# Optimization experiments

Measured on AMD Instinct MI355X. Metric: run time of the kernel, lower is better.

Reference implementation:

```python
import jax, jax.numpy as jnp
import numpy as np

B, N_IN, D_IN = 64, 2048, 16
N_OUT, D_OUT = 32, 32
ROUTINGS = 3
EPS = 1e-7


def squash(s, axis=-1):
    # standard CapsNet squash: s * ||s||^2 / (1 + ||s||^2) / ||s||
    sq_norm = jnp.sum(jnp.square(s), axis=axis, keepdims=True)
    scale = sq_norm / (1.0 + sq_norm) / jnp.sqrt(sq_norm + EPS)
    return s * scale


def setup_inputs() -> dict:
    key = jax.random.key(0)
    k1, k2 = jax.random.split(key)
    inputs = jax.random.normal(k1, (B, N_IN, D_IN), dtype=jnp.float32)
    # glorot-uniform-ish scale for [N_out, N_in, D_out, D_in] weight
    limit = np.sqrt(6.0 / (D_IN + D_OUT)).astype(np.float32)
    weight_matrix = jax.random.uniform(k2, (N_OUT, N_IN, D_OUT, D_IN), dtype=jnp.float32,
                                       minval=-limit, maxval=limit)
    return {"inputs": inputs, "weight_matrix": weight_matrix}


def reference(inputs, weight_matrix):
    # u_hat[b,o,i,d] = W[o,i,d,k] @ x[b,i,k]  (replaces tile + map_fn matmul)
    u_hat = jnp.einsum('oidk,bik->boid', weight_matrix, inputs)  # [B, N_out, N_in, D_out]
    b_logits = jnp.zeros((inputs.shape[0], N_OUT, 1, N_IN), dtype=u_hat.dtype)
    v = None
    for r in range(ROUTINGS):
        c = jax.nn.softmax(b_logits, axis=1)                      # softmax over output capsules
        s = jnp.einsum('boli,boid->bold', c, u_hat)               # [B, N_out, 1, D_out]
        v = squash(s)
        if r < ROUTINGS - 1:
            b_logits = b_logits + jnp.einsum('bold,boid->boli', v, u_hat)
    return jnp.squeeze(v, axis=2)                                 # [B, N_out, D_out]
```

## Files before the change

kernel.cpp:

```cpp
#include <hip/hip_runtime.h>

#define B_    64
#define NI    2048
#define DK    16
#define NO    32
#define DOUT  32
#define EPSQ  1e-7f

__device__ __forceinline__ unsigned pack2_bf16(float a, float b) {
    unsigned ua = __float_as_uint(a);
    unsigned ub = __float_as_uint(b);
    ua = (ua + 0x7fffu + ((ua >> 16) & 1u)) >> 16;
    ub = (ub + 0x7fffu + ((ub >> 16) & 1u)) >> 16;
    return ua | (ub << 16);
}
__device__ __forceinline__ float bf_lo(unsigned w) { return __uint_as_float(w << 16); }
__device__ __forceinline__ float bf_hi(unsigned w) { return __uint_as_float(w & 0xffff0000u); }


constexpr int WSTRIDE = 516;

__global__ __launch_bounds__(512)
void compute_uhat(const float* __restrict__ x, const float* __restrict__ W,
                  ushort* __restrict__ U)
{
    __shared__ float Ws[NO * WSTRIDE];
    __shared__ float xs[B_ * DK];
    const int i = blockIdx.x;
    const int t = threadIdx.x;

    if (t < 256) {
        const int b = t >> 2, k4 = t & 3;
        float4 v = *(const float4*)(x + ((size_t)b * NI + i) * DK + k4 * 4);
        *(float4*)&xs[b * DK + k4 * 4] = v;
    }

    #pragma unroll
    for (int jj = 0; jj < 8; ++jj) {
        const int p  = t + 512 * jj;
        const int oo = p >> 7;
        const int cc = p & 127;
        float4 v = ((const float4*)(W + ((size_t)oo * NI + i) * (DOUT * DK)))[cc];
        *(float4*)&Ws[oo * WSTRIDE + cc * 4] = v;
    }

    const int o  = t & 31;
    const int q  = (t >> 5) & 7;
    const int bh = t >> 8;

    __syncthreads();

    float w[64];
    {
        const float* wr = &Ws[o * WSTRIDE + q * 64];
        #pragma unroll
        for (int m = 0; m < 16; ++m) {
            float4 v = *(const float4*)(wr + 4 * m);
            w[4*m+0] = v.x; w[4*m+1] = v.y; w[4*m+2] = v.z; w[4*m+3] = v.w;
        }
    }

    const int j = q >> 1, half = q & 1;

    for (int bb = 0; bb < 32; ++bb) {
        const int b = bh * 32 + bb;
        const float4* xv = (const float4*)&xs[b * DK];
        const float4 x0 = xv[0], x1 = xv[1], x2 = xv[2], x3 = xv[3];

        float acc[4];
        #pragma unroll
        for (int dl = 0; dl < 4; ++dl) {
            const float* wr = &w[dl * 16];
            float a;
            a  = wr[0]  * x0.x + wr[1]  * x0.y + wr[2]  * x0.z + wr[3]  * x0.w;
            a += wr[4]  * x1.x + wr[5]  * x1.y + wr[6]  * x1.z + wr[7]  * x1.w;
            a += wr[8]  * x2.x + wr[9]  * x2.y + wr[10] * x2.z + wr[11] * x2.w;
            a += wr[12] * x3.x + wr[13] * x3.y + wr[14] * x3.z + wr[15] * x3.w;
            acc[dl] = a;
        }

        uint2 pk;
        pk.x = pack2_bf16(acc[0], acc[1]);
        pk.y = pack2_bf16(acc[2], acc[3]);
        const size_t off = ((((size_t)b * NI + i) * 4 + j) * NO + o) * 8 + half * 4;
        *(uint2*)(U + off) = pk;
    }
}

template<bool UNI>
__device__ __forceinline__ void proc_i(const uint4* cr, const float* vs, float* sacc)
{
    unsigned cw[16];
    #pragma unroll
    for (int jj = 0; jj < 4; ++jj) {
        cw[4*jj+0] = cr[jj].x; cw[4*jj+1] = cr[jj].y;
        cw[4*jj+2] = cr[jj].z; cw[4*jj+3] = cr[jj].w;
    }

    if (UNI) {
        #pragma unroll
        for (int m = 0; m < 16; ++m) {
            const int d0 = (m >> 2) * 8 + (m & 3) * 2;
            sacc[d0]     += bf_lo(cw[m]);
            sacc[d0 + 1] += bf_hi(cw[m]);
        }
    } else {
        float l0 = 0.f, l1 = 0.f, l2 = 0.f, l3 = 0.f;
        #pragma unroll
        for (int m = 0; m < 16; m += 4) {
            const int d0 = (m >> 2) * 8;
            l0 = fmaf(vs[d0+0], bf_lo(cw[m+0]), l0);
            l0 = fmaf(vs[d0+1], bf_hi(cw[m+0]), l0);
            l1 = fmaf(vs[d0+2], bf_lo(cw[m+1]), l1);
            l1 = fmaf(vs[d0+3], bf_hi(cw[m+1]), l1);
            l2 = fmaf(vs[d0+4], bf_lo(cw[m+2]), l2);
            l2 = fmaf(vs[d0+5], bf_hi(cw[m+2]), l2);
            l3 = fmaf(vs[d0+6], bf_lo(cw[m+3]), l3);
            l3 = fmaf(vs[d0+7], bf_hi(cw[m+3]), l3);
        }
        const float logit = (l0 + l1) + (l2 + l3);

        float mx = logit;
        #pragma unroll
        for (int msk = 16; msk >= 1; msk >>= 1) mx = fmaxf(mx, __shfl_xor(mx, msk));
        const float e = __expf(logit - mx);
        float ssum = e;
        #pragma unroll
        for (int msk = 16; msk >= 1; msk >>= 1) ssum += __shfl_xor(ssum, msk);
        const float c = e / ssum;

        #pragma unroll
        for (int m = 0; m < 16; ++m) {
            const int d0 = (m >> 2) * 8 + (m & 3) * 2;
            sacc[d0]     = fmaf(c, bf_lo(cw[m]), sacc[d0]);
            sacc[d0 + 1] = fmaf(c, bf_hi(cw[m]), sacc[d0 + 1]);
        }
    }
}

constexpr int BPB = 16;
constexpr int NIB = NI / BPB / 16;

template<bool UNI>
__global__ __launch_bounds__(256)
void routing_stream(const ushort* __restrict__ U, const float* __restrict__ Vsum,
                    float* __restrict__ s_out)
{
    __shared__ float sblk[NO * DOUT];
    const int t  = threadIdx.x;
    const int b  = blockIdx.x >> 4;
    const int i0 = (blockIdx.x & (BPB - 1)) * (NI / BPB);
    const int o  = t & 31;
    const int hw = t >> 5;

    for (int n = t; n < NO * DOUT; n += 256) sblk[n] = 0.f;

    float vs[DOUT];
    if (!UNI) {
        const float4* vp = (const float4*)(Vsum + ((size_t)b * NO + o) * DOUT);
        #pragma unroll
        for (int m = 0; m < 8; ++m) {
            float4 v = vp[m];
            vs[4*m+0] = v.x; vs[4*m+1] = v.y; vs[4*m+2] = v.z; vs[4*m+3] = v.w;
        }
    }
    float sacc[DOUT];
    #pragma unroll
    for (int d = 0; d < DOUT; ++d) sacc[d] = 0.f;

    __syncthreads();

    const uint4* up = (const uint4*)U + ((size_t)b * NI + i0 + 2 * hw) * (4 * NO) + o;
    const size_t step = (size_t)16 * 4 * NO;

    uint4 cur[8];
    #pragma unroll
    for (int jj = 0; jj < 4; ++jj) {
        cur[jj]     = up[jj * NO];
        cur[4 + jj] = up[4 * NO + jj * NO];
    }
    up += step;

    for (int ii = 0; ii < NIB; ++ii) {
        uint4 nxt[8];
        if (ii + 1 < NIB) {
            #pragma unroll
            for (int jj = 0; jj < 4; ++jj) {
                nxt[jj]     = up[jj * NO];
                nxt[4 + jj] = up[4 * NO + jj * NO];
            }
            up += step;
        }

        proc_i<UNI>(&cur[0], vs, sacc);
        proc_i<UNI>(&cur[4], vs, sacc);

        #pragma unroll
        for (int jj = 0; jj < 8; ++jj) cur[jj] = nxt[jj];
    }

    if (UNI) {
        #pragma unroll
        for (int d = 0; d < DOUT; ++d) sacc[d] *= 0.03125f;
    }

    #pragma unroll
    for (int d = 0; d < DOUT; ++d) sacc[d] += __shfl_xor(sacc[d], 32);

    if ((t & 32) == 0) {
        #pragma unroll
        for (int d = 0; d < DOUT; ++d) atomicAdd(&sblk[o * DOUT + d], sacc[d]);
    }
    __syncthreads();

    float* sp = s_out + (size_t)b * NO * DOUT;
    for (int n = t; n < NO * DOUT; n += 256) atomicAdd(&sp[n], sblk[n]);
}

__global__ __launch_bounds__(256)
void squash_update(const float* __restrict__ s, float* __restrict__ Vsum,
                   float* __restrict__ out, int last)
{
    const int tid  = threadIdx.x;
    const int pair = blockIdx.x * 8 + (tid >> 5);
    const int d    = tid & 31;
    const int idx  = pair * DOUT + d;

    const float val = s[idx];
    float sq = val * val;
    #pragma unroll
    for (int msk = 16; msk >= 1; msk >>= 1) sq += __shfl_xor(sq, msk);

    const float scale = sq / (1.f + sq) * rsqrtf(sq + EPSQ);
    const float v = val * scale;

    if (last) out[idx] = v;
    else      Vsum[idx] += v;
}

constexpr int BTILE  = 16;
constexpr int ITILE  = 32;
constexpr int CHUNKS = NI / ITILE;
constexpr int GB     = B_ / BTILE;
constexpr int WROW   = DOUT * DK + 4;

__global__ __launch_bounds__(512)
void routing_pass(const float* __restrict__ x, const float* __restrict__ W,
                  const float* __restrict__ Vsum, float* __restrict__ s_out)
{
    __shared__ float W_s[NO * WROW];
    const int tid   = threadIdx.x;
    const int o     = tid & 31;
    const int bl    = tid >> 5;
    const int chunk = blockIdx.x & (CHUNKS - 1);
    const int gb    = blockIdx.x / CHUNKS;
    const int b     = gb * BTILE + bl;

    float vs[DOUT];
    {
        const float4* vp = (const float4*)(Vsum + (size_t)(b * NO + o) * DOUT);
        #pragma unroll
        for (int qq = 0; qq < 8; ++qq) {
            float4 t2 = vp[qq];
            vs[4*qq+0] = t2.x; vs[4*qq+1] = t2.y; vs[4*qq+2] = t2.z; vs[4*qq+3] = t2.w;
        }
    }
    float sacc[DOUT];
    #pragma unroll
    for (int d = 0; d < DOUT; ++d) sacc[d] = 0.f;

    const int o_ld = tid >> 4;
    const int lpos = tid & 15;

    for (int ii = 0; ii < ITILE; ++ii) {
        const int i = chunk * ITILE + ii;
        __syncthreads();
        const float4* wsrc = (const float4*)W + ((size_t)o_ld * NI + i) * (DOUT * DK / 4);
        #pragma unroll
        for (int jj = 0; jj < 8; ++jj) {
            const int f4pos = lpos + 16 * jj;
            float4 v = wsrc[f4pos];
            *(float4*)&W_s[o_ld * WROW + f4pos * 4] = v;
        }
        __syncthreads();

        const float4* xg = (const float4*)(x + ((size_t)b * NI + i) * DK);
        const float4 xr0 = xg[0], xr1 = xg[1], xr2 = xg[2], xr3 = xg[3];

        float u[DOUT];
        float logit = 0.f;
        const float* wrow = &W_s[o * WROW];
        #pragma unroll
        for (int d = 0; d < DOUT; ++d) {
            const float4 w0 = *(const float4*)(wrow + d * DK + 0);
            const float4 w1 = *(const float4*)(wrow + d * DK + 4);
            const float4 w2 = *(const float4*)(wrow + d * DK + 8);
            const float4 w3 = *(const float4*)(wrow + d * DK + 12);
            float acc;
            acc  = w0.x * xr0.x + w0.y * xr0.y + w0.z * xr0.z + w0.w * xr0.w;
            acc += w1.x * xr1.x + w1.y * xr1.y + w1.z * xr1.z + w1.w * xr1.w;
            acc += w2.x * xr2.x + w2.y * xr2.y + w2.z * xr2.z + w2.w * xr2.w;
            acc += w3.x * xr3.x + w3.y * xr3.y + w3.z * xr3.z + w3.w * xr3.w;
            u[d]  = acc;
            logit = fmaf(vs[d], acc, logit);
        }

        float m = logit;
        #pragma unroll
        for (int msk = 16; msk >= 1; msk >>= 1) m = fmaxf(m, __shfl_xor(m, msk));
        const float e = __expf(logit - m);
        float ssum = e;
        #pragma unroll
        for (int msk = 16; msk >= 1; msk >>= 1) ssum += __shfl_xor(ssum, msk);
        const float c = e / ssum;

        #pragma unroll
        for (int d = 0; d < DOUT; ++d) sacc[d] = fmaf(c, u[d], sacc[d]);
    }

    float* sp = s_out + (size_t)(b * NO + o) * DOUT;
    #pragma unroll
    for (int d = 0; d < DOUT; ++d) atomicAdd(&sp[d], sacc[d]);
}

extern "C" void kernel_launch(void* const* d_in, const int* in_sizes, int n_in,
                              void* d_out, int out_size, void* d_ws, size_t ws_size,
                              hipStream_t stream)
{
    const float* x = (const float*)d_in[0];
    const float* W = (const float*)d_in[1];
    float* out = (float*)d_out;

    float* Vsum = (float*)d_ws;
    float* s    = Vsum + (size_t)B_ * NO * DOUT;
    ushort* U   = (ushort*)((char*)d_ws + 512 * 1024);

    const size_t need = 512 * 1024 + (size_t)B_ * NI * NO * DOUT * sizeof(ushort);

    hipMemsetAsync(Vsum, 0, (size_t)B_ * NO * DOUT * sizeof(float), stream);

    if (ws_size >= need) {
        compute_uhat<<<dim3(NI), dim3(512), 0, stream>>>(x, W, U);
        for (int r = 0; r < 3; ++r) {
            hipMemsetAsync(s, 0, (size_t)B_ * NO * DOUT * sizeof(float), stream);
            if (r == 0)
                routing_stream<true><<<dim3(B_ * BPB), dim3(256), 0, stream>>>(U, Vsum, s);
            else
                routing_stream<false><<<dim3(B_ * BPB), dim3(256), 0, stream>>>(U, Vsum, s);
            squash_update<<<dim3(B_ * NO / 8), dim3(256), 0, stream>>>(s, Vsum, out, r == 2);
        }
    } else {
        for (int r = 0; r < 3; ++r) {
            hipMemsetAsync(s, 0, (size_t)B_ * NO * DOUT * sizeof(float), stream);
            routing_pass<<<dim3(GB * CHUNKS), dim3(512), 0, stream>>>(x, W, Vsum, s);
            squash_update<<<dim3(B_ * NO / 8), dim3(256), 0, stream>>>(s, Vsum, out, r == 2);
        }
    }
}
```

Measured before the change: 459.0 us.

## Compute first routing pass directly from x and W, fuse squash into routing kernels

Adds a dedicated r0_sum kernel that computes the uniform-coefficient first routing sum straight from inputs and weights, so the bf16 u_hat buffer no longer has to be streamed an extra time for round 0. Squash and the v-sum accumulation move into the prologue of the routing kernels, which removes the separate squash_update launches and per-round memsets. Loads and stores of u_hat now use nontemporal hints, and the shared-memory atomic index is rotated to avoid bank conflicts. The cost is recomputing the W·x products in fp32 for round 0, which rereads the full W tensor, and every block now redundantly squashes all 32 capsules of its batch.

Result: slower. 739.8 us (+61.2%).

```diff
diff --git a/kernel.cpp b/kernel.cpp
--- a/kernel.cpp
+++ b/kernel.cpp
@@ -6,6 +6,9 @@
 #define NO    32
 #define DOUT  32
 #define EPSQ  1e-7f
+
+typedef unsigned u32x2 __attribute__((ext_vector_type(2)));
+typedef unsigned u32x4 __attribute__((ext_vector_type(4)));
 
 __device__ __forceinline__ unsigned pack2_bf16(float a, float b) {
     unsigned ua = __float_as_uint(a);
@@ -79,16 +82,77 @@
             acc[dl] = a;
         }
 
-        uint2 pk;
+        u32x2 pk;
         pk.x = pack2_bf16(acc[0], acc[1]);
         pk.y = pack2_bf16(acc[2], acc[3]);
         const size_t off = ((((size_t)b * NI + i) * 4 + j) * NO + o) * 8 + half * 4;
-        *(uint2*)(U + off) = pk;
-    }
-}
-
-template<bool UNI>
-__device__ __forceinline__ void proc_i(const uint4* cr, const float* vs, float* sacc)
+        __builtin_nontemporal_store(pk, (u32x2*)(U + off));
+    }
+}
+
+constexpr int R0_SEG = 8;
+constexpr int R0_IPB = NI / R0_SEG;
+constexpr int R0_CH  = 8;
+constexpr int XPAD   = 20;
+
+__global__ __launch_bounds__(512)
+void r0_sum(const float* __restrict__ x, const float* __restrict__ W,
+            float* __restrict__ s0)
+{
+    __shared__ float xs[R0_CH * B_ * XPAD];
+    const int o    = blockIdx.x & (NO - 1);
+    const int iseg = blockIdx.x >> 5;
+    const int t    = threadIdx.x;
+    const int b    = t & 63;
+    const int dq   = __builtin_amdgcn_readfirstlane(t >> 6);
+
+    float sacc[4] = {0.f, 0.f, 0.f, 0.f};
+
+    const int i0base = iseg * R0_IPB;
+    for (int c0 = 0; c0 < R0_IPB; c0 += R0_CH) {
+        const int ibase = i0base + c0;
+        __syncthreads();
+        #pragma unroll
+        for (int pp = 0; pp < 4; ++pp) {
+            const int p  = t + 512 * pp;
+            const int ii = p >> 8;
+            const int bb = (p >> 2) & 63;
+            const int m  = p & 3;
+            float4 v = *(const float4*)(x + ((size_t)bb * NI + ibase + ii) * DK + m * 4);
+            *(float4*)&xs[(ii * B_ + bb) * XPAD + m * 4] = v;
+        }
+        __syncthreads();
+
+        for (int ii = 0; ii < R0_CH; ++ii) {
+            const int i = ibase + ii;
+            const float* wr = W + ((size_t)o * NI + i) * (DOUT * DK) + dq * 64;
+            const float* xr = &xs[(ii * B_ + b) * XPAD];
+            const float4 x0 = *(const float4*)(xr + 0);
+            const float4 x1 = *(const float4*)(xr + 4);
+            const float4 x2 = *(const float4*)(xr + 8);
+            const float4 x3 = *(const float4*)(xr + 12);
+            #pragma unroll
+            for (int dl = 0; dl < 4; ++dl) {
+                const float4 w0 = *(const float4*)(wr + dl * 16 + 0);
+                const float4 w1 = *(const float4*)(wr + dl * 16 + 4);
+                const float4 w2 = *(const float4*)(wr + dl * 16 + 8);
+                const float4 w3 = *(const float4*)(wr + dl * 16 + 12);
+                float a;
+                a  = w0.x * x0.x + w0.y * x0.y + w0.z * x0.z + w0.w * x0.w;
+                a += w1.x * x1.x + w1.y * x1.y + w1.z * x1.z + w1.w * x1.w;
+                a += w2.x * x2.x + w2.y * x2.y + w2.z * x2.z + w2.w * x2.w;
+                a += w3.x * x3.x + w3.y * x3.y + w3.z * x3.z + w3.w * x3.w;
+                sacc[dl] += a;
+            }
+        }
+    }
+
+    #pragma unroll
+    for (int m = 0; m < 4; ++m)
+        atomicAdd(&s0[((size_t)b * NO + o) * DOUT + dq * 4 + m], sacc[m] * 0.03125f);
+}
+
+__device__ __forceinline__ void proc_one(const u32x4* cr, const float* vs, float* sacc)
 {
     unsigned cw[16];
     #pragma unroll
@@ -97,124 +161,148 @@
         cw[4*jj+2] = cr[jj].z; cw[4*jj+3] = cr[jj].w;
     }
 
-    if (UNI) {
-        #pragma unroll
-        for (int m = 0; m < 16; ++m) {
-            const int d0 = (m >> 2) * 8 + (m & 3) * 2;
-            sacc[d0]     += bf_lo(cw[m]);
-            sacc[d0 + 1] += bf_hi(cw[m]);
-        }
-    } else {
-        float l0 = 0.f, l1 = 0.f, l2 = 0.f, l3 = 0.f;
-        #pragma unroll
-        for (int m = 0; m < 16; m += 4) {
-            const int d0 = (m >> 2) * 8;
-            l0 = fmaf(vs[d0+0], bf_lo(cw[m+0]), l0);
-            l0 = fmaf(vs[d0+1], bf_hi(cw[m+0]), l0);
-            l1 = fmaf(vs[d0+2], bf_lo(cw[m+1]), l1);
-            l1 = fmaf(vs[d0+3], bf_hi(cw[m+1]), l1);
-            l2 = fmaf(vs[d0+4], bf_lo(cw[m+2]), l2);
-            l2 = fmaf(vs[d0+5], bf_hi(cw[m+2]), l2);
-            l3 = fmaf(vs[d0+6], bf_lo(cw[m+3]), l3);
-            l3 = fmaf(vs[d0+7], bf_hi(cw[m+3]), l3);
-        }
-        const float logit = (l0 + l1) + (l2 + l3);
-
-        float mx = logit;
-        #pragma unroll
-        for (int msk = 16; msk >= 1; msk >>= 1) mx = fmaxf(mx, __shfl_xor(mx, msk));
-        const float e = __expf(logit - mx);
-        float ssum = e;
-        #pragma unroll
-        for (int msk = 16; msk >= 1; msk >>= 1) ssum += __shfl_xor(ssum, msk);
-        const float c = e / ssum;
-
-        #pragma unroll
-        for (int m = 0; m < 16; ++m) {
-            const int d0 = (m >> 2) * 8 + (m & 3) * 2;
-            sacc[d0]     = fmaf(c, bf_lo(cw[m]), sacc[d0]);
-            sacc[d0 + 1] = fmaf(c, bf_hi(cw[m]), sacc[d0 + 1]);
-        }
+    float l0 = 0.f, l1 = 0.f, l2 = 0.f, l3 = 0.f;
+    #pragma unroll
+    for (int m = 0; m < 16; m += 4) {
+        const int d0 = (m >> 2) * 8;
+        l0 = fmaf(vs[d0+0], bf_lo(cw[m+0]), l0);
+        l0 = fmaf(vs[d0+1], bf_hi(cw[m+0]), l0);
+        l1 = fmaf(vs[d0+2], bf_lo(cw[m+1]), l1);
+        l1 = fmaf(vs[d0+3], bf_hi(cw[m+1]), l1);
+        l2 = fmaf(vs[d0+4], bf_lo(cw[m+2]), l2);
+        l2 = fmaf(vs[d0+5], bf_hi(cw[m+2]), l2);
+        l3 = fmaf(vs[d0+6], bf_lo(cw[m+3]), l3);
+        l3 = fmaf(vs[d0+7], bf_hi(cw[m+3]), l3);
+    }
+    const float logit = (l0 + l1) + (l2 + l3);
+
+    float mx = logit;
+    #pragma unroll
+    for (int msk = 16; msk >= 1; msk >>= 1) mx = fmaxf(mx, __shfl_xor(mx, msk));
+    const float e = __expf(logit - mx);
+    float ssum = e;
+    #pragma unroll
+    for (int msk = 16; msk >= 1; msk >>= 1) ssum += __shfl_xor(ssum, msk);
+    const float c = e / ssum;
+
+    #pragma unroll
+    for (int m = 0; m < 16; ++m) {
+        const int d0 = (m >> 2) * 8 + (m & 3) * 2;
+        sacc[d0]     = fmaf(c, bf_lo(cw[m]), sacc[d0]);
+        sacc[d0 + 1] = fmaf(c, bf_hi(cw[m]), sacc[d0 + 1]);
     }
 }
 
 constexpr int BPB = 16;
 constexpr int NIB = NI / BPB / 16;
 
-template<bool UNI>
+template<int R>
 __global__ __launch_bounds__(256)
-void routing_stream(const ushort* __restrict__ U, const float* __restrict__ Vsum,
-                    float* __restrict__ s_out)
+void routing_mid(const ushort* __restrict__ U, const float* __restrict__ sA,
+                 const float* __restrict__ sB, float* __restrict__ s_out)
 {
     __shared__ float sblk[NO * DOUT];
+    __shared__ float vsh[NO][DOUT + 1];
     const int t  = threadIdx.x;
     const int b  = blockIdx.x >> 4;
     const int i0 = (blockIdx.x & (BPB - 1)) * (NI / BPB);
+
+    {
+        const int oo = t >> 3;
+        const int dg = t & 7;
+        float4 sv = *(const float4*)(sA + ((size_t)b * NO + oo) * DOUT + dg * 4);
+        float sq = sv.x*sv.x + sv.y*sv.y + sv.z*sv.z + sv.w*sv.w;
+        #pragma unroll
+        for (int msk = 4; msk >= 1; msk >>= 1) sq += __shfl_xor(sq, msk);
+        float sc = sq / (1.f + sq) * rsqrtf(sq + EPSQ);
+        float v0 = sv.x * sc, v1 = sv.y * sc, v2 = sv.z * sc, v3 = sv.w * sc;
+        if (R == 2) {
+            float4 s2v = *(const float4*)(sB + ((size_t)b * NO + oo) * DOUT + dg * 4);
+            float sq2 = s2v.x*s2v.x + s2v.y*s2v.y + s2v.z*s2v.z + s2v.w*s2v.w;
+            #pragma unroll
+            for (int msk = 4; msk >= 1; msk >>= 1) sq2 += __shfl_xor(sq2, msk);
+            float sc2 = sq2 / (1.f + sq2) * rsqrtf(sq2 + EPSQ);
+            v0 += s2v.x * sc2; v1 += s2v.y * sc2; v2 += s2v.z * sc2; v3 += s2v.w * sc2;
+        }
+        vsh[oo][dg*4+0] = v0; vsh[oo][dg*4+1] = v1;
+        vsh[oo][dg*4+2] = v2; vsh[oo][dg*4+3] = v3;
+    }
+    for (int n = t; n < NO * DOUT; n += 256) sblk[n] = 0.f;
+    __syncthreads();
+
     const int o  = t & 31;
     const int hw = t >> 5;
 
-    for (int n = t; n < NO * DOUT; n += 256) sblk[n] = 0.f;
-
     float vs[DOUT];
-    if (!UNI) {
-        const float4* vp = (const float4*)(Vsum + ((size_t)b * NO + o) * DOUT);
-        #pragma unroll
-        for (int m = 0; m < 8; ++m) {
-            float4 v = vp[m];
-            vs[4*m+0] = v.x; vs[4*m+1] = v.y; vs[4*m+2] = v.z; vs[4*m+3] = v.w;
-        }
-    }
+    #pragma unroll
+    for (int d = 0; d < DOUT; ++d) vs[d] = vsh[o][d];
+
     float sacc[DOUT];
     #pragma unroll
     for (int d = 0; d < DOUT; ++d) sacc[d] = 0.f;
 
-    __syncthreads();
-
-    const uint4* up = (const uint4*)U + ((size_t)b * NI + i0 + 2 * hw) * (4 * NO) + o;
+    const u32x4* up = (const u32x4*)U + ((size_t)b * NI + i0 + 2 * hw) * (4 * NO) + o;
     const size_t step = (size_t)16 * 4 * NO;
 
-    uint4 cur[8];
+    u32x4 cur[8];
     #pragma unroll
     for (int jj = 0; jj < 4; ++jj) {
-        cur[jj]     = up[jj * NO];
-        cur[4 + jj] = up[4 * NO + jj * NO];
+        cur[jj]     = __builtin_nontemporal_load(up + jj * NO);
+        cur[4 + jj] = __builtin_nontemporal_load(up + 4 * NO + jj * NO);
     }
     up += step;
 
     for (int ii = 0; ii < NIB; ++ii) {
-        uint4 nxt[8];
+        u32x4 nxt[8];
         if (ii + 1 < NIB) {
             #pragma unroll
             for (int jj = 0; jj < 4; ++jj) {
-                nxt[jj]     = up[jj * NO];
-                nxt[4 + jj] = up[4 * NO + jj * NO];
+                nxt[jj]     = __builtin_nontemporal_load(up + jj * NO);
+                nxt[4 + jj] = __builtin_nontemporal_load(up + 4 * NO + jj * NO);
             }
             up += step;
         }
 
-        proc_i<UNI>(&cur[0], vs, sacc);
-        proc_i<UNI>(&cur[4], vs, sacc);
+        proc_one(&cur[0], vs, sacc);
+        proc_one(&cur[4], vs, sacc);
 
         #pragma unroll
         for (int jj = 0; jj < 8; ++jj) cur[jj] = nxt[jj];
     }
 
-    if (UNI) {
-        #pragma unroll
-        for (int d = 0; d < DOUT; ++d) sacc[d] *= 0.03125f;
-    }
-
     #pragma unroll
     for (int d = 0; d < DOUT; ++d) sacc[d] += __shfl_xor(sacc[d], 32);
 
     if ((t & 32) == 0) {
         #pragma unroll
-        for (int d = 0; d < DOUT; ++d) atomicAdd(&sblk[o * DOUT + d], sacc[d]);
+        for (int d = 0; d < DOUT; ++d)
+            atomicAdd(&sblk[o * DOUT + ((d + o) & 31)], sacc[d]);
     }
     __syncthreads();
 
     float* sp = s_out + (size_t)b * NO * DOUT;
-    for (int n = t; n < NO * DOUT; n += 256) atomicAdd(&sp[n], sblk[n]);
+    for (int n = t; n < NO * DOUT; n += 256) {
+        const int oo = n >> 5, ds = n & 31;
+        const int dd = (ds - oo) & 31;
+        atomicAdd(&sp[oo * DOUT + dd], sblk[n]);
+    }
+}
+
+__global__ __launch_bounds__(256)
+void squash_final(const float* __restrict__ s, float* __restrict__ out)
+{
+    const int tid  = threadIdx.x;
+    const int pair = blockIdx.x * 8 + (tid >> 5);
+    const int d    = tid & 31;
+    const int idx  = pair * DOUT + d;
+
+    const float val = s[idx];
+    float sq = val * val;
+    #pragma unroll
+    for (int msk = 16; msk >= 1; msk >>= 1) sq += __shfl_xor(sq, msk);
+
+    const float scale = sq / (1.f + sq) * rsqrtf(sq + EPSQ);
+    out[idx] = val * scale;
 }
 
 __global__ __launch_bounds__(256)
@@ -331,29 +419,27 @@
     const float* W = (const float*)d_in[1];
     float* out = (float*)d_out;
 
-    float* Vsum = (float*)d_ws;
-    float* s    = Vsum + (size_t)B_ * NO * DOUT;
-    ushort* U   = (ushort*)((char*)d_ws + 512 * 1024);
-
-    const size_t need = 512 * 1024 + (size_t)B_ * NI * NO * DOUT * sizeof(ushort);
-
-    hipMemsetAsync(Vsum, 0, (size_t)B_ * NO * DOUT * sizeof(float), stream);
+    float* s0 = (float*)d_ws;
+    float* s1 = s0 + (size_t)B_ * NO * DOUT;
+    float* s2 = s1 + (size_t)B_ * NO * DOUT;
+    ushort* U = (ushort*)((char*)d_ws + (1 << 20));
+
+    const size_t need = (1 << 20) + (size_t)B_ * NI * NO * DOUT * sizeof(ushort);
+
+    hipMemsetAsync(d_ws, 0, (size_t)3 * B_ * NO * DOUT * sizeof(float), stream);
 
     if (ws_size >= need) {
+        r0_sum<<<dim3(NO * R0_SEG), dim3(512), 0, stream>>>(x, W, s0);
         compute_uhat<<<dim3(NI), dim3(512), 0, stream>>>(x, W, U);
-        for (int r = 0; r < 3; ++r) {
-            hipMemsetAsync(s, 0, (size_t)B_ * NO * DOUT * sizeof(float), stream);
-            if (r == 0)
-                routing_stream<true><<<dim3(B_ * BPB), dim3(256), 0, stream>>>(U, Vsum, s);
-            else
-                routing_stream<false><<<dim3(B_ * BPB), dim3(256), 0, stream>>>(U, Vsum, s);
-            squash_update<<<dim3(B_ * NO / 8), dim3(256), 0, stream>>>(s, Vsum, out, r == 2);
-        }
+        routing_mid<1><<<dim3(B_ * BPB), dim3(256), 0, stream>>>(U, s0, s0, s1);
+        routing_mid<2><<<dim3(B_ * BPB), dim3(256), 0, stream>>>(U, s0, s1, s2);
+        squash_final<<<dim3(B_ * NO / 8), dim3(256), 0, stream>>>(s2, out);
     } else {
         for (int r = 0; r < 3; ++r) {
-            hipMemsetAsync(s, 0, (size_t)B_ * NO * DOUT * sizeof(float), stream);
-            routing_pass<<<dim3(GB * CHUNKS), dim3(512), 0, stream>>>(x, W, Vsum, s);
-            squash_update<<<dim3(B_ * NO / 8), dim3(256), 0, stream>>>(s, Vsum, out, r == 2);
-        }
-    }
-}
+            if (r > 0)
+                hipMemsetAsync(s0, 0, (size_t)B_ * NO * DOUT * sizeof(float), stream);
+            routing_pass<<<dim3(GB * CHUNKS), dim3(512), 0, stream>>>(x, W, s1, s0);
+            squash_update<<<dim3(B_ * NO / 8), dim3(256), 0, stream>>>(s0, s1, out, r == 2);
+        }
+    }
+}
```
